# Kernel tuning notes

Hardware: AMD Instinct MI355X
Metric: run time of the kernel (lower is better)

Reference implementation:

```python
import jax, jax.numpy as jnp
import numpy as np
from jax import lax

B, L = 2, 2048
DIM, HEADS = 1024, 16
HD = DIM // HEADS            # 64
D_STATE, D_CONV = 16, 4
D_INNER = 2 * DIM            # mamba expand=2
DT_RANK = DIM // 16          # 64


def setup_inputs() -> dict:
    key = jax.random.key(0)
    ks = jax.random.split(key, 12)
    w = lambda k, shape, s=0.02: (jax.random.normal(k, shape, jnp.float32) * s)
    # A initialized as in Mamba: A_log = log(1..d_state) per channel
    A_log = jnp.log(jnp.tile(jnp.arange(1, D_STATE + 1, dtype=jnp.float32), (D_INNER, 1)))
    return {
        "x": jax.random.normal(ks[0], (B, L, DIM), jnp.float32),
        # MultiQueryAttention params (Wqkv: dim -> dim + 2*head_dim)
        "wqkv": w(ks[1], (DIM, DIM + 2 * HD)),
        "bqkv": jnp.zeros((DIM + 2 * HD,), jnp.float32),
        "w_attn_out": w(ks[2], (DIM, DIM)),
        "b_attn_out": jnp.zeros((DIM,), jnp.float32),
        # MambaBlock params
        "w_in": w(ks[3], (DIM, 2 * D_INNER)),          # in_proj (no bias)
        "conv_w": w(ks[4], (D_INNER, D_CONV), 0.1),    # depthwise causal conv
        "conv_b": jnp.zeros((D_INNER,), jnp.float32),
        "w_xproj": w(ks[5], (D_INNER, DT_RANK + 2 * D_STATE)),
        "w_dt": w(ks[6], (DT_RANK, D_INNER)),
        "b_dt": w(ks[7], (D_INNER,), 0.01),
        "A_log": A_log,
        "Dp": jnp.ones((D_INNER,), jnp.float32),
        "w_out": w(ks[8], (D_INNER, DIM)),             # out_proj (no bias)
    }


def _mqa(x, wqkv, bqkv, w_attn_out, b_attn_out):
    b, l, d = x.shape
    qkv = x @ wqkv + bqkv
    q = qkv[..., :DIM].reshape(b, l, HEADS, HD)          # blhd
    k = qkv[..., DIM:DIM + HD]                           # bmd (single shared head)
    v = qkv[..., DIM + HD:]                              # bmd
    scores = jnp.einsum("blhd,bmd->bhlm", q, k) / np.sqrt(HD).astype(np.float32)
    causal = jnp.tril(jnp.ones((l, l), bool))
    scores = jnp.where(causal, scores, jnp.finfo(scores.dtype).min)
    attn = jax.nn.softmax(scores, axis=-1)
    out = jnp.einsum("bhlm,bmd->blhd", attn, v).reshape(b, l, DIM)
    return out @ w_attn_out + b_attn_out


def _mamba(x, w_in, conv_w, conv_b, w_xproj, w_dt, b_dt, A_log, Dp, w_out):
    b, l, d = x.shape
    xr = x @ w_in                                        # (b,l,2*d_inner)
    u0, res = xr[..., :D_INNER], xr[..., D_INNER:]
    # causal depthwise conv1d (torch pads d_conv-1 both sides then slices [:l])
    lhs = u0.transpose(0, 2, 1)                          # (b, d_inner, l)
    rhs = conv_w[:, None, :]                             # (d_inner, 1, d_conv)
    xc = lax.conv_general_dilated(
        lhs, rhs, window_strides=(1,), padding=[(D_CONV - 1, 0)],
        dimension_numbers=("NCH", "OIH", "NCH"), feature_group_count=D_INNER)
    u = jax.nn.silu((xc + conv_b[None, :, None]).transpose(0, 2, 1))  # (b,l,d_inner)

    x_dbl = u @ w_xproj
    delta = jax.nn.softplus(x_dbl[..., :DT_RANK] @ w_dt + b_dt)       # (b,l,d_inner)
    Bm = x_dbl[..., DT_RANK:DT_RANK + D_STATE]                        # (b,l,n)
    Cm = x_dbl[..., DT_RANK + D_STATE:]                               # (b,l,n)
    A = -jnp.exp(A_log)                                               # (d_inner, n)

    def step(h, inp):
        d_t, b_t, c_t, u_t = inp                       # (b,d),(b,n),(b,n),(b,d)
        dA = jnp.exp(d_t[..., None] * A)               # (b,d,n)
        h = dA * h + (d_t * u_t)[..., None] * b_t[:, None, :]
        y = jnp.einsum("bdn,bn->bd", h, c_t)
        return h, y

    xs = (delta.transpose(1, 0, 2), Bm.transpose(1, 0, 2),
          Cm.transpose(1, 0, 2), u.transpose(1, 0, 2))
    h0 = jnp.zeros((b, D_INNER, D_STATE), u.dtype)
    _, ys = lax.scan(step, h0, xs)                     # (l,b,d_inner)
    y = ys.transpose(1, 0, 2) + u * Dp
    y = y * jax.nn.silu(res)
    return y @ w_out


def reference(x, wqkv, bqkv, w_attn_out, b_attn_out, w_in, conv_w, conv_b,
              w_xproj, w_dt, b_dt, A_log, Dp, w_out):
    attended = _mqa(x, wqkv, bqkv, w_attn_out, b_attn_out)
    x1 = attended + x                                   # residual 1
    y = _mamba(x1, w_in, conv_w, conv_b, w_xproj, w_dt, b_dt, A_log, Dp, w_out)
    return y + x1                                       # residual 2
```

## Files before the change

kernel.cpp:

```cpp
#include <hip/hip_runtime.h>

#define L_SEQ   2048
#define BATCH   2
#define NDIM    1024
#define NHEADS  16
#define HD      64
#define DSTATE  16
#define DCONV   4
#define DINNER  2048
#define DTRANK  64
#define CHUNK   32
#define NCHUNK  (L_SEQ / CHUNK)
#define SPLIT_KT 8
#define LOG2E   1.4426950408889634f

typedef short  short8  __attribute__((ext_vector_type(8)));
typedef float  floatx4 __attribute__((ext_vector_type(4)));

#define AS1 __attribute__((address_space(1)))
#define AS3 __attribute__((address_space(3)))

__device__ __forceinline__ float bf2f(ushort u) {
    union { uint i; float f; } v; v.i = ((uint)u) << 16; return v.f;
}
#if defined(__has_builtin) && __has_builtin(__builtin_amdgcn_cvt_pk_bf16_f32)
__device__ __forceinline__ ushort f2bf(float f) {
    auto p = __builtin_amdgcn_cvt_pk_bf16_f32(f, f);
    union { decltype(p) v; ushort u[2]; } cv; cv.v = p;
    return cv.u[0];
}
__device__ __forceinline__ uint pk2bf(float lo, float hi) {
    auto p = __builtin_amdgcn_cvt_pk_bf16_f32(lo, hi);
    union { decltype(p) v; uint u; } cv; cv.v = p;
    return cv.u;
}
#else
__device__ __forceinline__ ushort f2bf(float f) {
    uint x = __float_as_uint(f);
    uint r = (x + 0x7fffu + ((x >> 16) & 1u)) >> 16;
    return (ushort)r;
}
__device__ __forceinline__ uint pk2bf(float lo, float hi) {
    return ((uint)f2bf(hi) << 16) | (uint)f2bf(lo);
}
#endif
#if defined(__has_builtin) && __has_builtin(__builtin_amdgcn_exp2f)
__device__ __forceinline__ float fast_exp2(float x) {
    return __builtin_amdgcn_exp2f(x);
}
#else
__device__ __forceinline__ float fast_exp2(float x) {
    return __expf(x * 0.6931471805599453f);
}
#endif
__device__ __forceinline__ float silu_f(float x) {
    return x / (1.f + __expf(-x));
}
__device__ __forceinline__ void gld_lds16(const void* g, void* l) {
    __builtin_amdgcn_global_load_lds((const AS1 uint*)g, (AS3 uint*)l, 16, 0, 0);
}
__device__ __forceinline__ float cvt_one(const void* s, int i, int f) {
    return f ? ((const float*)s)[i] : bf2f(((const ushort*)s)[i]);
}

__global__ __launch_bounds__(256) void prep_kernel(
    const void* __restrict__ x_raw,
    const void* __restrict__ wqkv, const void* __restrict__ wao,
    const void* __restrict__ win,  const void* __restrict__ wxp,
    const void* __restrict__ wdt,  const void* __restrict__ wout,
    const void* __restrict__ bqkv, const void* __restrict__ bao,
    const void* __restrict__ convw, const void* __restrict__ convb,
    const void* __restrict__ bdt,  const void* __restrict__ Alog,
    const void* __restrict__ Dp,
    ushort* __restrict__ x_b, ushort* __restrict__ wqkv_t,
    ushort* __restrict__ wao_t, ushort* __restrict__ win_t,
    ushort* __restrict__ wxp_t, ushort* __restrict__ wdt_t,
    ushort* __restrict__ wout_t,
    float* __restrict__ bqkv_f, float* __restrict__ bao_f,
    float* __restrict__ convw_f, float* __restrict__ convb_f,
    float* __restrict__ bdt_f, float* __restrict__ Alog_f,
    float* __restrict__ Dp_f, int* __restrict__ flag)
{
    __shared__ int cnt;
    __shared__ float tile[32][33];
    if (threadIdx.x == 0) cnt = 0;
    __syncthreads();
    {
        ushort w = ((const ushort*)x_raw)[threadIdx.x];
        int e = (w >> 7) & 0xff;
        if (w != 0 && (e < 100 || e > 140)) atomicAdd(&cnt, 1);
    }
    __syncthreads();
    const int f = (cnt >= 16) ? 1 : 0;
    if (blockIdx.x == 0 && threadIdx.x == 0) *flag = f;

    int id = blockIdx.x;
    if (id < 16384) {
        int i = id * 256 + threadIdx.x;
        x_b[i] = f2bf(cvt_one(x_raw, i, f));
        return;
    }
    id -= 16384;

    const void* src = nullptr; ushort* dst = nullptr; int K = 0, N = 0;
    if (id < 1152)                     { src = wqkv; dst = wqkv_t; K = 1024; N = 1152; }
    else if ((id -= 1152) < 1024)      { src = wao;  dst = wao_t;  K = 1024; N = 1024; }
    else if ((id -= 1024) < 4096)      { src = win;  dst = win_t;  K = 1024; N = 4096; }
    else if ((id -= 4096) < 192)       { src = wxp;  dst = wxp_t;  K = 2048; N = 96;   }
    else if ((id -= 192)  < 128)       { src = wdt;  dst = wdt_t;  K = 64;   N = 2048; }
    else if ((id -= 128)  < 2048)      { src = wout; dst = wout_t; K = 2048; N = 1024; }
    else {
        id -= 2048;
        if (id < 256) {
            wxp_t[(size_t)96 * DINNER + id * 256 + threadIdx.x] = 0;
        } else {
            int i = (id - 256) * 256 + threadIdx.x;
            if      (i < 1152)   bqkv_f[i]          = cvt_one(bqkv,  i,          f);
            else if (i < 2176)   bao_f[i - 1152]    = cvt_one(bao,   i - 1152,   f);
            else if (i < 10368)  convw_f[i - 2176]  = cvt_one(convw, i - 2176,   f);
            else if (i < 12416)  convb_f[i - 10368] = cvt_one(convb, i - 10368,  f);
            else if (i < 14464)  bdt_f[i - 12416]   = cvt_one(bdt,   i - 12416,  f);
            else if (i < 47232) {
                int ai = i - 14464;
                float v = -__expf(cvt_one(Alog, ai, f)) * LOG2E;
                Alog_f[ai] = v;
                int np1 = (ai & 15) + 1;
                float expv = -(float)np1 * LOG2E;
                if (fabsf(v - expv) > 1e-5f * (float)np1)
                    atomicAdd(flag + 1, 1);
            }
            else if (i < 49280)  Dp_f[i - 47232]    = cvt_one(Dp,    i - 47232,  f);
        }
        return;
    }

    const int ntn = N / 32;
    const int n0 = (id % ntn) * 32, k0 = (id / ntn) * 32;
    const int tx = threadIdx.x & 31, ty = threadIdx.x >> 5;
    #pragma unroll
    for (int r = 0; r < 4; ++r) {
        size_t o = (size_t)(k0 + ty + r * 8) * N + n0 + tx;
        tile[ty + r * 8][tx] = cvt_one(src, (int)o, f);
    }
    __syncthreads();
    #pragma unroll
    for (int r = 0; r < 4; ++r) {
        int n = n0 + ty + r * 8;
        dst[(size_t)n * K + k0 + tx] = f2bf(tile[tx][ty + r * 8]);
    }
}

__global__ __launch_bounds__(256) void gemm128(
    const ushort* __restrict__ A, int lda,
    const ushort* __restrict__ Wt,
    const float* __restrict__ bias,
    const ushort* __restrict__ resb,
    ushort* __restrict__ outb, float* __restrict__ outf,
    const int* __restrict__ dtflag,
    int N, int K, int act, int klen, float* __restrict__ psum, int swap)
{
    __shared__ __align__(16) char smem[65536];

    const int tid  = threadIdx.x;
    const int wave = tid >> 6;
    const int lane = tid & 63;
    const int wm = (wave >> 1) * 64;
    const int wn = (wave & 1) * 64;
    const int fm = lane & 15;
    const int quad = lane >> 4;

    int bx = blockIdx.x, by = blockIdx.y;
    {
        const int gx = gridDim.x;
        const int nwg = gx * gridDim.y;
        const int id = by * gx + bx;
        const int qq = nwg >> 3;
        const int sid = (id & 7) * qq + (id >> 3);
        bx = sid % gx; by = sid / gx;
    }
    const int m0 = (swap ? bx : by) * 128;
    const int n0 = (swap ? by : bx) * 128;

    floatx4 acc[4][4];
    #pragma unroll
    for (int i = 0; i < 4; ++i)
        #pragma unroll
        for (int j = 0; j < 4; ++j) acc[i][j] = (floatx4){0.f, 0.f, 0.f, 0.f};

    int rowv[4], kgv[4];
    #pragma unroll
    for (int j = 0; j < 4; ++j) {
        int c = wave * 256 + j * 64 + lane;
        rowv[j] = c >> 3;
        kgv[j]  = (((c & 7) ^ ((c >> 3) & 7))) * 8;
    }

    const int kbeg = psum ? (blockIdx.z * klen) : 0;
    const int kend = kbeg + klen;

    auto stage = [&](int buf, int k0) {
        ushort* As = (ushort*)(smem + buf * 32768);
        ushort* Bs = (ushort*)(smem + buf * 32768 + 16384);
        #pragma unroll
        for (int j = 0; j < 4; ++j)
            gld_lds16(A  + (size_t)(m0 + rowv[j]) * lda + k0 + kgv[j],
                      &As[(wave * 256 + j * 64) * 8]);
        #pragma unroll
        for (int j = 0; j < 4; ++j)
            gld_lds16(Wt + (size_t)(n0 + rowv[j]) * K   + k0 + kgv[j],
                      &Bs[(wave * 256 + j * 64) * 8]);
    };

    stage(0, kbeg);
    __syncthreads();

    int cur = 0;
    for (int k0 = kbeg; k0 < kend; k0 += 64) {
        if (k0 + 64 < kend) stage(cur ^ 1, k0 + 64);
        const ushort* As = (const ushort*)(smem + cur * 32768);
        const ushort* Bs = (const ushort*)(smem + cur * 32768 + 16384);

        #pragma unroll
        for (int h = 0; h < 2; ++h) {
            short8 af[4], bf[4];
            #pragma unroll
            for (int i = 0; i < 4; ++i) {
                int row = wm + i * 16 + fm;
                int slot = (h * 4 + quad) ^ (row & 7);
                af[i] = *(const short8*)&As[row * 64 + slot * 8];
            }
            #pragma unroll
            for (int j = 0; j < 4; ++j) {
                int row = wn + j * 16 + fm;
                int slot = (h * 4 + quad) ^ (row & 7);
                bf[j] = *(const short8*)&Bs[row * 64 + slot * 8];
            }
            #pragma unroll
            for (int i = 0; i < 4; ++i)
                #pragma unroll
                for (int j = 0; j < 4; ++j)
                    acc[i][j] = __builtin_amdgcn_mfma_f32_16x16x32_bf16(af[i], bf[j], acc[i][j], 0, 0, 0);
        }
        __syncthreads();
        cur ^= 1;
    }

    if (psum) {
        int mgrid = swap ? gridDim.x : gridDim.y;
        float* po = psum + (size_t)blockIdx.z * ((size_t)mgrid * 128) * N;
        #pragma unroll
        for (int j = 0; j < 4; ++j) {
            int col = n0 + wn + j * 16 + fm;
            #pragma unroll
            for (int i = 0; i < 4; ++i) {
                int rowb = m0 + wm + i * 16 + quad * 4;
                #pragma unroll
                for (int r = 0; r < 4; ++r)
                    po[(size_t)(rowb + r) * N + col] = acc[i][j][r];
            }
        }
        return;
    }

    const int flagv = dtflag ? *dtflag : 0;
    const bool wf = dtflag ? (flagv != 0) : (outf != nullptr);
    float* Cs = (float*)smem;
    const int lrw = (wm >> 1) + quad * 4;
    #pragma unroll
    for (int p = 0; p < 2; ++p) {
        #pragma unroll
        for (int ih = 0; ih < 2; ++ih) {
            const int i = 2 * p + ih;
            #pragma unroll
            for (int j = 0; j < 4; ++j) {
                float bvv = bias ? bias[n0 + wn + j * 16 + fm] : 0.f;
                #pragma unroll
                for (int r = 0; r < 4; ++r) {
                    float v = acc[i][j][r] + bvv;
                    if (act == 1)
                        v = fmaxf(v, 0.f) + __logf(1.f + __expf(-fabsf(v)));
                    Cs[(lrw + ih * 16 + r) * 132 + wn + j * 16 + fm] = v;
                }
            }
        }
        __syncthreads();
        #pragma unroll
        for (int g = 0; g < 4; ++g) {
            const int lr   = g * 16 + (tid >> 4);
            const int colc = (tid & 15) * 8;
            const int grow = m0 + (lr >> 5) * 64 + (2 * p + ((lr >> 4) & 1)) * 16 + (lr & 15);
            const size_t o = (size_t)grow * N + n0 + colc;
            floatx4 v0 = *(const floatx4*)&Cs[lr * 132 + colc];
            floatx4 v1 = *(const floatx4*)&Cs[lr * 132 + colc + 4];
            float vv[8] = {v0[0], v0[1], v0[2], v0[3], v1[0], v1[1], v1[2], v1[3]};
            if (resb) {
                short8 rs = *(const short8*)&resb[o];
                #pragma unroll
                for (int k = 0; k < 8; ++k) vv[k] += bf2f((ushort)rs[k]);
            }
            if (wf) {
                *(floatx4*)&outf[o]     = (floatx4){vv[0], vv[1], vv[2], vv[3]};
                *(floatx4*)&outf[o + 4] = (floatx4){vv[4], vv[5], vv[6], vv[7]};
            } else {
                short8 ov;
                #pragma unroll
                for (int k = 0; k < 8; ++k) ov[k] = (short)f2bf(vv[k]);
                *(short8*)&outb[o] = ov;
            }
        }
        __syncthreads();
    }
}

__global__ __launch_bounds__(256) void combine_xdbl(
    const float* __restrict__ psum, ushort* __restrict__ xdbl)
{
    int idx = blockIdx.x * 256 + threadIdx.x;
    int row = idx / 96, col = idx - row * 96;
    float s = 0.f;
    #pragma unroll
    for (int z = 0; z < 8; ++z)
        s += psum[(size_t)z * 4096 * 128 + row * 128 + col];
    xdbl[idx] = f2bf(s);
}

__global__ __launch_bounds__(256) void flash_attn_split(
    const ushort* __restrict__ qkv, ushort* __restrict__ att,
    ushort* __restrict__ partO, float* __restrict__ partL)
{
    __shared__ __align__(16) ushort Ks[64 * 72];
    __shared__ __align__(16) ushort Vt[64 * 72];

    const int id  = blockIdx.x;
    const int e   = id >> 3;
    const int hgb = id & 7;
    const int hg  = hgb >> 1;
    const int b   = hgb & 1;
    int tile, s;
    if (e < 104) {
        if      (e < 50)  { s = 0; tile = 63 - e; }
        else if (e < 84)  { s = 1; tile = 63 - (e - 50); }
        else if (e < 102) { s = 2; tile = 63 - (e - 84); }
        else              { s = 3; tile = 63 - (e - 102); }
    } else {
        const int rem = e - 104;
        const int w   = 7 - (rem >> 3);
        s    = (rem & 7) >> 1;
        tile = 2 * (8 * s + w) - 2 + (rem & 1);
    }

    const int q0 = tile * 32;
    const int nkv = (q0 >> 6) + 1;
    const int nsplit = (nkv + SPLIT_KT - 1) / SPLIT_KT;
    const int kt0 = s * SPLIT_KT;
    const int kt1 = (nkv < kt0 + SPLIT_KT) ? nkv : (kt0 + SPLIT_KT);

    const int tid  = threadIdx.x;
    const int wave = tid >> 6;
    const int lane = tid & 63;
    const int fm   = lane & 15;
    const int quad = lane >> 4;
    const int h    = hg * 4 + wave;

    const int srow = tid >> 3;
    const int scol = (tid & 7) * 8;
    const int vsw  = (tid & 7) << 3;

    const int addrA = (fm + (quad & 1) * 32) * 4;
    const int addrB = addrA + 64;
    const bool jlo_sel = (quad < 2);

    short8 qf[2][2];
    #pragma unroll
    for (int i = 0; i < 2; ++i)
        #pragma unroll
        for (int kh = 0; kh < 2; ++kh)
            qf[i][kh] = *(const short8*)(qkv +
                (size_t)(b * L_SEQ + q0 + i * 16 + fm) * 1152 + h * HD + kh * 32 + quad * 8);

    floatx4 acc[2][4];
    float l_lane[2];
    #pragma unroll
    for (int i = 0; i < 2; ++i) {
        #pragma unroll
        for (int j = 0; j < 4; ++j) acc[i][j] = (floatx4){0.f, 0.f, 0.f, 0.f};
        l_lane[i] = 0.f;
    }

    short8 kreg[2], vreg[2];
    {
        const int kv0 = kt0 * 64;
        #pragma unroll
        for (int pass = 0; pass < 2; ++pass) {
            int row = srow + pass * 32;
            const ushort* kp = qkv + (size_t)(b * L_SEQ + kv0 + row) * 1152 + NDIM + scol;
            kreg[pass] = *(const short8*)kp;
            vreg[pass] = *(const short8*)(kp + HD);
        }
    }

    for (int kt = kt0; kt < kt1; ++kt) {
        const int kv0 = kt * 64;
        __syncthreads();
        #pragma unroll
        for (int pass = 0; pass < 2; ++pass) {
            int row = srow + pass * 32;
            *(short8*)&Ks[row * 72 + scol] = kreg[pass];
            int mw = row ^ vsw;
            #pragma unroll
            for (int i2 = 0; i2 < 8; ++i2) Vt[(scol + i2) * 72 + mw] = (ushort)vreg[pass][i2];
        }
        __syncthreads();

        if (kt + 1 < kt1) {
            const int kv0n = (kt + 1) * 64;
            #pragma unroll
            for (int pass = 0; pass < 2; ++pass) {
                int row = srow + pass * 32;
                const ushort* kp = qkv + (size_t)(b * L_SEQ + kv0n + row) * 1152 + NDIM + scol;
                kreg[pass] = *(const short8*)kp;
                vreg[pass] = *(const short8*)(kp + HD);
            }
        }

        floatx4 spT[4][2];
        __builtin_amdgcn_s_setprio(1);
        #pragma unroll
        for (int j = 0; j < 4; ++j) {
            short8 kf0 = *(const short8*)&Ks[(j * 16 + fm) * 72 + quad * 8];
            short8 kf1 = *(const short8*)&Ks[(j * 16 + fm) * 72 + 32 + quad * 8];
            #pragma unroll
            for (int i = 0; i < 2; ++i) {
                floatx4 z = (floatx4){0.f, 0.f, 0.f, 0.f};
                z = __builtin_amdgcn_mfma_f32_16x16x32_bf16(kf0, qf[i][0], z, 0, 0, 0);
                z = __builtin_amdgcn_mfma_f32_16x16x32_bf16(kf1, qf[i][1], z, 0, 0, 0);
                spT[j][i] = z;
            }
        }
        __builtin_amdgcn_s_setprio(0);

        const bool diag = (kt == nkv - 1);
        #pragma unroll
        for (int j = 0; j < 4; ++j)
            #pragma unroll
            for (int i = 0; i < 2; ++i) {
                #pragma unroll
                for (int r = 0; r < 4; ++r) {
                    float p = fast_exp2(spT[j][i][r] * 0.18033688011112042f);
                    if (diag) {
                        int kvg = kv0 + j * 16 + quad * 4 + r;
                        int qg  = q0 + i * 16 + fm;
                        if (kvg > qg) p = 0.f;
                    }
                    spT[j][i][r] = p;
                    l_lane[i] += p;
                }
            }

        uint w0[4][2], w1[4][2];
        #pragma unroll
        for (int j = 0; j < 4; ++j)
            #pragma unroll
            for (int i = 0; i < 2; ++i) {
                w0[j][i] = pk2bf(spT[j][i][0], spT[j][i][1]);
                w1[j][i] = pk2bf(spT[j][i][2], spT[j][i][3]);
            }

        short8 pf[2][2];
        #pragma unroll
        for (int i = 0; i < 2; ++i)
            #pragma unroll
            for (int kh = 0; kh < 2; ++kh) {
                const int jl = kh * 2, jh = kh * 2 + 1;
                uint a0 = (uint)__builtin_amdgcn_ds_bpermute(addrA, (int)w0[jl][i]);
                uint a1 = (uint)__builtin_amdgcn_ds_bpermute(addrA, (int)w0[jh][i]);
                uint b0 = (uint)__builtin_amdgcn_ds_bpermute(addrA, (int)w1[jl][i]);
                uint b1 = (uint)__builtin_amdgcn_ds_bpermute(addrA, (int)w1[jh][i]);
                uint c0 = (uint)__builtin_amdgcn_ds_bpermute(addrB, (int)w0[jl][i]);
                uint c1 = (uint)__builtin_amdgcn_ds_bpermute(addrB, (int)w0[jh][i]);
                uint d0 = (uint)__builtin_amdgcn_ds_bpermute(addrB, (int)w1[jl][i]);
                uint d1 = (uint)__builtin_amdgcn_ds_bpermute(addrB, (int)w1[jh][i]);
                union { uint u[4]; short8 s; } cv;
                cv.u[0] = jlo_sel ? a0 : a1;
                cv.u[1] = jlo_sel ? b0 : b1;
                cv.u[2] = jlo_sel ? c0 : c1;
                cv.u[3] = jlo_sel ? d0 : d1;
                pf[i][kh] = cv.s;
            }

        __builtin_amdgcn_s_setprio(1);
        #pragma unroll
        for (int dj = 0; dj < 4; ++dj) {
            int d = dj * 16 + fm;
            int sw8 = ((d >> 3) & 7) << 3;
            short8 vf0 = *(const short8*)&Vt[d * 72 + ((quad * 8) ^ sw8)];
            short8 vf1 = *(const short8*)&Vt[d * 72 + ((32 + quad * 8) ^ sw8)];
            #pragma unroll
            for (int i = 0; i < 2; ++i) {
                acc[i][dj] = __builtin_amdgcn_mfma_f32_16x16x32_bf16(pf[i][0], vf0, acc[i][dj], 0, 0, 0);
                acc[i][dj] = __builtin_amdgcn_mfma_f32_16x16x32_bf16(pf[i][1], vf1, acc[i][dj], 0, 0, 0);
            }
        }
        __builtin_amdgcn_s_setprio(0);
    }

    #pragma unroll
    for (int i = 0; i < 2; ++i) {
        float rs = l_lane[i];
        rs += __shfl_xor(rs, 16);
        rs += __shfl_xor(rs, 32);
        l_lane[i] = rs;
    }

    if (nsplit == 1) {
        #pragma unroll
        for (int i = 0; i < 2; ++i) {
            float inv[4];
            #pragma unroll
            for (int r = 0; r < 4; ++r)
                inv[r] = 1.f / __shfl(l_lane[i], quad * 4 + r, 16);
            #pragma unroll
            for (int dj = 0; dj < 4; ++dj)
                #pragma unroll
                for (int r = 0; r < 4; ++r) {
                    int q = q0 + i * 16 + quad * 4 + r;
                    att[(size_t)(b * L_SEQ + q) * NDIM + h * HD + dj * 16 + fm] =
                        f2bf(acc[i][dj][r] * inv[r]);
                }
        }
    } else {
        size_t pbase = ((size_t)((s * 2 + b) * 16 + h)) * L_SEQ;
        #pragma unroll
        for (int i = 0; i < 2; ++i)
            #pragma unroll
            for (int dj = 0; dj < 4; ++dj)
                #pragma unroll
                for (int r = 0; r < 4; ++r) {
                    int q = q0 + i * 16 + quad * 4 + r;
                    partO[(pbase + q) * 64 + dj * 16 + fm] = f2bf(acc[i][dj][r]);
                }
        if (lane < 16) {
            #pragma unroll
            for (int i = 0; i < 2; ++i)
                partL[pbase + q0 + i * 16 + fm] = l_lane[i];
        }
    }
}

__global__ __launch_bounds__(256) void attn_combine(
    const ushort* __restrict__ partO, const float* __restrict__ partL,
    ushort* __restrict__ att)
{
    int gid = blockIdx.x * 256 + threadIdx.x;
    int t8 = gid & 7;
    int row = gid >> 3;
    int q  = 512 + (row % 1536);
    int bh = row / 1536;
    int b = bh >> 4, h = bh & 15;
    int nsplit = (((q >> 5) >> 1) + 1 + SPLIT_KT - 1) / SPLIT_KT;

    float sum[8] = {0.f, 0.f, 0.f, 0.f, 0.f, 0.f, 0.f, 0.f};
    float L = 0.f;
    for (int s = 0; s < nsplit; ++s) {
        size_t pbase = ((size_t)((s * 2 + b) * 16 + h)) * L_SEQ + q;
        L += partL[pbase];
        short8 o = *(const short8*)&partO[pbase * 64 + t8 * 8];
        #pragma unroll
        for (int k = 0; k < 8; ++k) sum[k] += bf2f((ushort)o[k]);
    }
    float inv = 1.f / L;
    short8 outv;
    #pragma unroll
    for (int k = 0; k < 8; ++k) outv[k] = (short)f2bf(sum[k] * inv);
    *(short8*)&att[((size_t)(b * L_SEQ + q)) * NDIM + h * HD + t8 * 8] = outv;
}

__global__ __launch_bounds__(256) void conv_silu(
    const ushort* __restrict__ xr, const float* __restrict__ conv_w,
    const float* __restrict__ conv_b, ushort* __restrict__ u)
{
    const int c   = ((blockIdx.x & 7) << 8) + threadIdx.x;
    const int bl0 = (blockIdx.x >> 3) << 4;
    const int l0  = bl0 & (L_SEQ - 1);

    const floatx4 wv = *(const floatx4*)&conv_w[c * DCONV];
    const float bias = conv_b[c];

    float xv[19];
    #pragma unroll
    for (int t = 0; t < 19; ++t) {
        int ls = l0 - 3 + t;
        xv[t] = (ls >= 0)
              ? bf2f(xr[(size_t)(bl0 - 3 + t) * (2 * DINNER) + c])
              : 0.f;
    }

    #pragma unroll
    for (int t = 0; t < 16; ++t) {
        float a = bias + xv[t] * wv[0] + xv[t + 1] * wv[1]
                       + xv[t + 2] * wv[2] + xv[t + 3] * wv[3];
        u[(size_t)(bl0 + t) * DINNER + c] = f2bf(silu_f(a));
    }
}

__global__ __launch_bounds__(256) void scan_phase1(
    const ushort* __restrict__ delta, const ushort* __restrict__ u,
    const ushort* __restrict__ xdbl, const float* __restrict__ negA,
    float* __restrict__ Hend, float* __restrict__ Sdt,
    const int* __restrict__ sflag)
{
    const int idx  = blockIdx.x * 256 + threadIdx.x;
    const int lane = idx & 63;
    const int g    = idx >> 6;
    const int half = lane >> 5;
    const int d    = ((g & 63) << 5) + (lane & 31);
    const int b    = (g >> 6) & (BATCH - 1);
    const int c    = g >> 7;
    const int strA = (sflag[1] == 0);

    float h[8];
    #pragma unroll
    for (int n = 0; n < 8; ++n) h[n] = 0.f;

    const int t0 = c * CHUNK;
    size_t bd = ((size_t)b * L_SEQ + t0) * DINNER + d;
    size_t bx = ((size_t)b * L_SEQ + t0) * 96 + DTRANK + half * 8;
    float sdt = 0.f;

    if (strA) {
        for (int t = 0; t < CHUNK; ++t) {
            float dt = bf2f(delta[bd]);
            float uv = bf2f(u[bd]);
            sdt += dt;
            float du = dt * uv;
            short8 B0 = *(const short8*)&xdbl[bx];
            float w  = fast_exp2(-dt * LOG2E);
            float w2 = w * w, w4 = w2 * w2, w8 = w4 * w4;
            float p3 = w2 * w;
            float q[8] = {w, w2, p3, w4, w4 * w, w4 * w2, w4 * p3, w8};
            float sc = half ? w8 : 1.f;
            #pragma unroll
            for (int n = 0; n < 8; ++n)
                h[n] = (q[n] * sc) * h[n] + du * bf2f((ushort)B0[n]);
            bd += DINNER; bx += 96;
        }
    } else {
        float Av[8];
        #pragma unroll
        for (int n = 0; n < 8; ++n)
            Av[n] = negA[d * DSTATE + half * 8 + n];
        for (int t = 0; t < CHUNK; ++t) {
            float dt = bf2f(delta[bd]);
            float uv = bf2f(u[bd]);
            sdt += dt;
            float du = dt * uv;
            short8 B0 = *(const short8*)&xdbl[bx];
            #pragma unroll
            for (int n = 0; n < 8; ++n)
                h[n] = fast_exp2(dt * Av[n]) * h[n] + du * bf2f((ushort)B0[n]);
            bd += DINNER; bx += 96;
        }
    }

    size_t ho = (((size_t)c * BATCH + b) * DINNER + d) * DSTATE + half * 8;
    *(floatx4*)&Hend[ho]     = (floatx4){h[0], h[1], h[2], h[3]};
    *(floatx4*)&Hend[ho + 4] = (floatx4){h[4], h[5], h[6], h[7]};
    if (half == 0)
        Sdt[((size_t)c * BATCH + b) * DINNER + d] = sdt;
}

__global__ __launch_bounds__(256) void scan_phase2(
    float* __restrict__ H, const float* __restrict__ Sdt,
    const float* __restrict__ negA)
{
    const int idx = blockIdx.x * 256 + threadIdx.x;
    const int n = idx & (DSTATE - 1);
    const int d = (idx >> 4) & (DINNER - 1);
    const int b = idx >> 15;

    const float Av = negA[d * DSTATE + n];
    const size_t hstride = (size_t)BATCH * DINNER * DSTATE;
    const size_t sstride = (size_t)BATCH * DINNER;
    const size_t ho0 = ((size_t)b * DINNER + d) * DSTATE + n;
    const size_t so0 = (size_t)b * DINNER + d;

    float hin = 0.f;
    for (int c0 = 0; c0 < NCHUNK; c0 += 8) {
        float e[8], dAc[8];
        #pragma unroll
        for (int k = 0; k < 8; ++k) {
            e[k]   = H[ho0 + (size_t)(c0 + k) * hstride];
            dAc[k] = Sdt[so0 + (size_t)(c0 + k) * sstride];
        }
        #pragma unroll
        for (int k = 0; k < 8; ++k) dAc[k] = fast_exp2(Av * dAc[k]);
        #pragma unroll
        for (int k = 0; k < 8; ++k) {
            H[ho0 + (size_t)(c0 + k) * hstride] = hin;
            hin = dAc[k] * hin + e[k];
        }
    }
}

__global__ __launch_bounds__(256) void scan_phase3(
    const ushort* __restrict__ delta, const ushort* __restrict__ u,
    const ushort* __restrict__ xdbl, const float* __restrict__ negA,
    const float* __restrict__ Hin, const float* __restrict__ Dp,
    const ushort* __restrict__ xr, ushort* __restrict__ yb,
    const int* __restrict__ sflag)
{
    const int idx = blockIdx.x * 256 + threadIdx.x;
    const int d = idx & (DINNER - 1);
    const int b = (idx >> 11) & (BATCH - 1);
    const int c = idx >> 12;
    const int strA = (sflag[1] == 0);

    float h[DSTATE];
    size_t ho = (((size_t)c * BATCH + b) * DINNER + d) * DSTATE;
    #pragma unroll
    for (int n = 0; n < DSTATE; n += 4) {
        floatx4 hv = *(const floatx4*)&Hin[ho + n];
        h[n] = hv[0]; h[n + 1] = hv[1]; h[n + 2] = hv[2]; h[n + 3] = hv[3];
    }

    const float Dpd = Dp[d];
    const int t0 = c * CHUNK;
    size_t bd = ((size_t)b * L_SEQ + t0) * DINNER + d;
    size_t bx = ((size_t)b * L_SEQ + t0) * 96 + DTRANK;
    size_t br = ((size_t)b * L_SEQ + t0) * (2 * DINNER) + DINNER + d;

    if (strA) {
        for (int t = 0; t < CHUNK; ++t) {
            float dt = bf2f(delta[bd]);
            float uv = bf2f(u[bd]);
            float du = dt * uv;
            short8 B0 = *(const short8*)&xdbl[bx];
            short8 B1 = *(const short8*)&xdbl[bx + 8];
            short8 C0 = *(const short8*)&xdbl[bx + 16];
            short8 C1 = *(const short8*)&xdbl[bx + 24];
            float w  = fast_exp2(-dt * LOG2E);
            float w2 = w * w, w4 = w2 * w2, w8 = w4 * w4;
            float p3 = w2 * w, p5 = w4 * w, p6 = w4 * w2, p7 = w4 * p3;
            float dA[16] = {w, w2, p3, w4, p5, p6, p7, w8,
                            w8 * w, w8 * w2, w8 * p3, w8 * w4,
                            w8 * p5, w8 * p6, w8 * p7, w8 * w8};
            float y = 0.f;
            #pragma unroll
            for (int n = 0; n < 8; ++n) {
                h[n] = dA[n] * h[n] + du * bf2f((ushort)B0[n]);
                y += h[n] * bf2f((ushort)C0[n]);
            }
            #pragma unroll
            for (int n = 0; n < 8; ++n) {
                h[8 + n] = dA[8 + n] * h[8 + n] + du * bf2f((ushort)B1[n]);
                y += h[8 + n] * bf2f((ushort)C1[n]);
            }
            float yv = y + uv * Dpd;
            float r  = bf2f(xr[br]);
            yb[bd] = f2bf(yv * silu_f(r));
            bd += DINNER; bx += 96; br += 2 * DINNER;
        }
    } else {
        float Av[DSTATE];
        #pragma unroll
        for (int n = 0; n < DSTATE; ++n)
            Av[n] = negA[d * DSTATE + n];
        for (int t = 0; t < CHUNK; ++t) {
            float dt = bf2f(delta[bd]);
            float uv = bf2f(u[bd]);
            float du = dt * uv;
            short8 B0 = *(const short8*)&xdbl[bx];
            short8 B1 = *(const short8*)&xdbl[bx + 8];
            short8 C0 = *(const short8*)&xdbl[bx + 16];
            short8 C1 = *(const short8*)&xdbl[bx + 24];
            float y = 0.f;
            #pragma unroll
            for (int n = 0; n < 8; ++n) {
                h[n] = fast_exp2(dt * Av[n]) * h[n] + du * bf2f((ushort)B0[n]);
                y += h[n] * bf2f((ushort)C0[n]);
            }
            #pragma unroll
            for (int n = 0; n < 8; ++n) {
                h[8 + n] = fast_exp2(dt * Av[8 + n]) * h[8 + n] + du * bf2f((ushort)B1[n]);
                y += h[8 + n] * bf2f((ushort)C1[n]);
            }
            float yv = y + uv * Dpd;
            float r  = bf2f(xr[br]);
            yb[bd] = f2bf(yv * silu_f(r));
            bd += DINNER; bx += 96; br += 2 * DINNER;
        }
    }
}

extern "C" void kernel_launch(void* const* d_in, const int* in_sizes, int n_in,
                              void* d_out, int out_size, void* d_ws, size_t ws_size,
                              hipStream_t stream) {
    const void* x_raw      = d_in[0];
    const void* wqkv_raw   = d_in[1];
    const void* bqkv_raw   = d_in[2];
    const void* wao_raw    = d_in[3];
    const void* bao_raw    = d_in[4];
    const void* win_raw    = d_in[5];
    const void* convw_raw  = d_in[6];
    const void* convb_raw  = d_in[7];
    const void* wxp_raw    = d_in[8];
    const void* wdt_raw    = d_in[9];
    const void* bdt_raw    = d_in[10];
    const void* Alog_raw   = d_in[11];
    const void* Dp_raw     = d_in[12];
    const void* wout_raw   = d_in[13];

    const int M = BATCH * L_SEQ;

    char* p = (char*)d_ws;
    size_t off = 0;
    auto A_ = [&](size_t bytes) { void* q = p + off; off += (bytes + 255) & ~255ull; return q; };

    ushort* x_b    = (ushort*)A_((size_t)M * NDIM * 2);
    ushort* wqkv_t = (ushort*)A_((size_t)NDIM * 1152 * 2);
    ushort* wao_t  = (ushort*)A_((size_t)NDIM * NDIM * 2);
    ushort* win_t  = (ushort*)A_((size_t)NDIM * 4096 * 2);
    float*  psum   = (float*)x_b;
    ushort* yb     = x_b;
    float*  Sdt    = (float*)(x_b + (size_t)M * DINNER);

    ushort* qkv    = (ushort*)A_((size_t)M * 1152 * 2);
    ushort* att    = (ushort*)A_((size_t)M * NDIM * 2);
    float*  Hend   = (float*)qkv;

    ushort* delta_b = (ushort*)A_((size_t)M * DINNER * 2);

    ushort* wxp_t  = (ushort*)A_((size_t)128 * DINNER * 2);
    ushort* wdt_t  = (ushort*)A_((size_t)DTRANK * DINNER * 2);
    ushort* wout_t = (ushort*)A_((size_t)DINNER * NDIM * 2);
    float*  bqkv_f = (float*)A_(1152 * 4);
    float*  bao_f  = (float*)A_(NDIM * 4);
    float*  convw_f= (float*)A_((size_t)DINNER * DCONV * 4);
    float*  convb_f= (float*)A_(DINNER * 4);
    float*  bdt_f  = (float*)A_(DINNER * 4);
    float*  Alog_f = (float*)A_((size_t)DINNER * DSTATE * 4);
    float*  Dp_f   = (float*)A_(DINNER * 4);
    int*    flag   = (int*)A_(256);
    ushort* x1b    = (ushort*)A_((size_t)M * NDIM * 2);
    ushort* xr     = (ushort*)A_((size_t)M * 4096 * 2);
    ushort* u      = (ushort*)A_((size_t)M * DINNER * 2);
    ushort* xdbl   = (ushort*)A_((size_t)M * 96 * 2);

    ushort* partO = xr;
    float*  partL = (float*)u;

    dim3 blk(256);

    hipMemsetAsync(flag, 0, 8, stream);

    prep_kernel<<<dim3(25473), blk, 0, stream>>>(
        x_raw, wqkv_raw, wao_raw, win_raw, wxp_raw, wdt_raw, wout_raw,
        bqkv_raw, bao_raw, convw_raw, convb_raw, bdt_raw, Alog_raw, Dp_raw,
        x_b, wqkv_t, wao_t, win_t, wxp_t, wdt_t, wout_t,
        bqkv_f, bao_f, convw_f, convb_f, bdt_f, Alog_f, Dp_f, flag);

    gemm128<<<dim3(1152 / 128, M / 128), blk, 0, stream>>>(
        x_b, NDIM, wqkv_t, bqkv_f, nullptr, qkv, nullptr, nullptr, 1152, NDIM, 0, NDIM, nullptr, 0);

    flash_attn_split<<<dim3(1280), blk, 0, stream>>>(
        qkv, att, partO, partL);
    attn_combine<<<dim3(1536), blk, 0, stream>>>(partO, partL, att);

    gemm128<<<dim3(NDIM / 128, M / 128), blk, 0, stream>>>(
        att, NDIM, wao_t, bao_f, x_b, x1b, nullptr, nullptr, NDIM, NDIM, 0, NDIM, nullptr, 0);

    gemm128<<<dim3(M / 128, 4096 / 128), blk, 0, stream>>>(
        x1b, NDIM, win_t, nullptr, nullptr, xr, nullptr, nullptr, 4096, NDIM, 0, NDIM, nullptr, 1);

    conv_silu<<<dim3((M / 16) * (DINNER / 256)), blk, 0, stream>>>(xr, convw_f, convb_f, u);

    gemm128<<<dim3(1, M / 128, 8), blk, 0, stream>>>(
        u, DINNER, wxp_t, nullptr, nullptr, nullptr, nullptr, nullptr, 128, DINNER, 0, DINNER / 8, psum, 0);
    combine_xdbl<<<dim3(M * 96 / 256), blk, 0, stream>>>(psum, xdbl);

    gemm128<<<dim3(DINNER / 128, M / 128), blk, 0, stream>>>(
        xdbl, 96, wdt_t, bdt_f, nullptr, delta_b, nullptr, nullptr, DINNER, DTRANK, 1, DTRANK, nullptr, 0);

    scan_phase1<<<dim3(NCHUNK * BATCH * DINNER * 2 / 256), blk, 0, stream>>>(
        delta_b, u, xdbl, Alog_f, Hend, Sdt, flag);
    scan_phase2<<<dim3(BATCH * DINNER * DSTATE / 256), blk, 0, stream>>>(
        Hend, Sdt, Alog_f);
    scan_phase3<<<dim3(NCHUNK * BATCH * DINNER / 256), blk, 0, stream>>>(
        delta_b, u, xdbl, Alog_f, Hend, Dp_f, xr, yb, flag);

    gemm128<<<dim3(M / 128, NDIM / 128), blk, 0, stream>>>(
        yb, DINNER, wout_t, nullptr, x1b, (ushort*)d_out, (float*)d_out, flag, NDIM, DINNER, 0, DINNER, nullptr, 1);
}
```

Measured before the change: 396.3 us.

## Double-buffer K/V tiles in flash attention and store V row-major

The flash attention kernel now keeps K and V in two LDS buffers, with global loads issued two tiles ahead. This cuts the per-iteration barriers from two to one. V is no longer transposed into LDS with scalar scattered stores. It is written row-major with vector stores under an XOR swizzle, and the PV step gathers the transposed fragments with eight scalar LDS reads per fragment. The aim is to overlap staging with compute and cheapen the V store, at the cost of more LDS use, extra register pressure, and more LDS read instructions in the inner MMA loop.

```diff
diff --git a/kernel.cpp b/kernel.cpp
--- a/kernel.cpp
+++ b/kernel.cpp
@@ -328,8 +328,8 @@
     const ushort* __restrict__ qkv, ushort* __restrict__ att,
     ushort* __restrict__ partO, float* __restrict__ partL)
 {
-    __shared__ __align__(16) ushort Ks[64 * 72];
-    __shared__ __align__(16) ushort Vt[64 * 72];
+    __shared__ __align__(16) ushort Ks[2][64 * 72];
+    __shared__ __align__(16) ushort Vs[2][64 * 64];
 
     const int id  = blockIdx.x;
     const int e   = id >> 3;
@@ -364,7 +364,6 @@
 
     const int srow = tid >> 3;
     const int scol = (tid & 7) * 8;
-    const int vsw  = (tid & 7) << 3;
 
     const int addrA = (fm + (quad & 1) * 32) * 4;
     const int addrB = addrA + 64;
@@ -388,47 +387,43 @@
     }
 
     short8 kreg[2], vreg[2];
-    {
-        const int kv0 = kt0 * 64;
+    auto loadkv = [&](int kt_) {
+        const int kv0n = kt_ * 64;
         #pragma unroll
         for (int pass = 0; pass < 2; ++pass) {
             int row = srow + pass * 32;
-            const ushort* kp = qkv + (size_t)(b * L_SEQ + kv0 + row) * 1152 + NDIM + scol;
+            const ushort* kp = qkv + (size_t)(b * L_SEQ + kv0n + row) * 1152 + NDIM + scol;
             kreg[pass] = *(const short8*)kp;
             vreg[pass] = *(const short8*)(kp + HD);
         }
-    }
-
+    };
+    auto stagebuf = [&](int bufi) {
+        #pragma unroll
+        for (int pass = 0; pass < 2; ++pass) {
+            int row = srow + pass * 32;
+            *(short8*)&Ks[bufi][row * 72 + scol] = kreg[pass];
+            int sc2 = scol ^ (((row >> 3) & 3) << 4);
+            *(short8*)&Vs[bufi][row * 64 + sc2] = vreg[pass];
+        }
+    };
+
+    loadkv(kt0);
+    stagebuf(0);
+    if (kt0 + 1 < kt1) loadkv(kt0 + 1);
+    __syncthreads();
+
+    int cur = 0;
     for (int kt = kt0; kt < kt1; ++kt) {
         const int kv0 = kt * 64;
-        __syncthreads();
-        #pragma unroll
-        for (int pass = 0; pass < 2; ++pass) {
-            int row = srow + pass * 32;
-            *(short8*)&Ks[row * 72 + scol] = kreg[pass];
-            int mw = row ^ vsw;
-            #pragma unroll
-            for (int i2 = 0; i2 < 8; ++i2) Vt[(scol + i2) * 72 + mw] = (ushort)vreg[pass][i2];
-        }
-        __syncthreads();
-
-        if (kt + 1 < kt1) {
-            const int kv0n = (kt + 1) * 64;
-            #pragma unroll
-            for (int pass = 0; pass < 2; ++pass) {
-                int row = srow + pass * 32;
-                const ushort* kp = qkv + (size_t)(b * L_SEQ + kv0n + row) * 1152 + NDIM + scol;
-                kreg[pass] = *(const short8*)kp;
-                vreg[pass] = *(const short8*)(kp + HD);
-            }
-        }
+        if (kt + 1 < kt1) stagebuf(cur ^ 1);
+        if (kt + 2 < kt1) loadkv(kt + 2);
 
         floatx4 spT[4][2];
         __builtin_amdgcn_s_setprio(1);
         #pragma unroll
         for (int j = 0; j < 4; ++j) {
-            short8 kf0 = *(const short8*)&Ks[(j * 16 + fm) * 72 + quad * 8];
-            short8 kf1 = *(const short8*)&Ks[(j * 16 + fm) * 72 + 32 + quad * 8];
+            short8 kf0 = *(const short8*)&Ks[cur][(j * 16 + fm) * 72 + quad * 8];
+            short8 kf1 = *(const short8*)&Ks[cur][(j * 16 + fm) * 72 + 32 + quad * 8];
             #pragma unroll
             for (int i = 0; i < 2; ++i) {
                 floatx4 z = (floatx4){0.f, 0.f, 0.f, 0.f};
@@ -491,10 +486,15 @@
         __builtin_amdgcn_s_setprio(1);
         #pragma unroll
         for (int dj = 0; dj < 4; ++dj) {
-            int d = dj * 16 + fm;
-            int sw8 = ((d >> 3) & 7) << 3;
-            short8 vf0 = *(const short8*)&Vt[d * 72 + ((quad * 8) ^ sw8)];
-            short8 vf1 = *(const short8*)&Vt[d * 72 + ((32 + quad * 8) ^ sw8)];
+            const int dx = (dj * 16 + fm) ^ (quad << 4);
+            ushort t0[8], t1[8];
+            #pragma unroll
+            for (int e2 = 0; e2 < 8; ++e2) {
+                t0[e2] = Vs[cur][(quad * 8 + e2) * 64 + dx];
+                t1[e2] = Vs[cur][(32 + quad * 8 + e2) * 64 + dx];
+            }
+            short8 vf0 = *(short8*)t0;
+            short8 vf1 = *(short8*)t1;
             #pragma unroll
             for (int i = 0; i < 2; ++i) {
                 acc[i][dj] = __builtin_amdgcn_mfma_f32_16x16x32_bf16(pf[i][0], vf0, acc[i][dj], 0, 0, 0);
@@ -502,6 +502,9 @@
             }
         }
         __builtin_amdgcn_s_setprio(0);
+
+        __syncthreads();
+        cur ^= 1;
     }
 
     #pragma unroll
```

Result: slower. 414.4 us (+4.6%).
